# Kernel optimization log

Measured on AMD Instinct MI355X. Metric: run time of the kernel, lower is better.

The kernel has to match this reference:

```python
import jax, jax.numpy as jnp
import numpy as np

IN_C, OUT_C, K, STRIDE, PAD = 16, 32, 3, 1, 1


def setup_inputs() -> dict:
    key = jax.random.key(0)
    kx, kw = jax.random.split(key)
    x = jax.random.normal(kx, (2, IN_C, 8, 8, 32, 32), dtype=jnp.float32)
    # matches torch.randn init of nn.Parameter
    weight = jax.random.normal(kw, (OUT_C, IN_C, K, K, K, K), dtype=jnp.float32)
    bias = jnp.zeros((OUT_C,), dtype=jnp.float32)
    return {"x": x, "weight": weight, "bias": bias}


def _conv4d(x, weight):
    # 4 spatial dims; layout N C T D H W, weight O I kT kD kH kW.
    dn = jax.lax.ConvDimensionNumbers(
        lhs_spec=(0, 1, 2, 3, 4, 5),
        rhs_spec=(0, 1, 2, 3, 4, 5),
        out_spec=(0, 1, 2, 3, 4, 5),
    )
    return jax.lax.conv_general_dilated(
        x, weight,
        window_strides=(STRIDE,) * 4,
        padding=((PAD, PAD),) * 4,
        dimension_numbers=dn,
    )


def reference(x, weight, bias):
    # Same math as unfold(im2col) + matmul + bias in the torch module,
    # expressed as a single N-D convolution (implicit GEMM).
    out = _conv4d(x, weight)  # [B, out_c, oT, oD, oH, oW]
    return out + bias[None, :, None, None, None, None]
```

## Files before the change

### kernel.cpp

```cpp
#include <hip/hip_runtime.h>

#define IN_C  16
#define OUT_C 32
#define NB 2
#define TT 8
#define DD 8
#define HH 32
#define WW 32
#define TP 10
#define DP 10
#define HP 34
#define WPAD 34

#define XT_ROW_B  1088
#define XT_ELEMS  (NB*TP*DP*HP*2*WPAD*8)
#define WT_TAPS_P 84
#define WT_ELEMS  (WT_TAPS_P*2*OUT_C*8)

#define A_SLAB_B 12288
#define B_CHUNK_B 28672

typedef __bf16 bf16x8 __attribute__((ext_vector_type(8)));
typedef float  f32x4  __attribute__((ext_vector_type(4)));
typedef float  f32x16 __attribute__((ext_vector_type(16)));

__device__ __forceinline__ unsigned short f2bf(float f) {
    unsigned int u = __builtin_bit_cast(unsigned int, f);
    u += 0x7fffu + ((u >> 16) & 1u);
    return (unsigned short)(u >> 16);
}

__device__ __forceinline__ void gload16(const void* g, void* l) {
    __builtin_amdgcn_global_load_lds(
        (const __attribute__((address_space(1))) unsigned int*)g,
        (__attribute__((address_space(3))) unsigned int*)l, 16, 0, 0);
}

__global__ __launch_bounds__(256) void prep_kernel(const float* __restrict__ x,
                                                   const float* __restrict__ wsrc,
                                                   unsigned short* __restrict__ xt,
                                                   unsigned short* __restrict__ wt) {
    int b = blockIdx.x;
    int tid = threadIdx.x;
    if (b < 4096) {
        __shared__ unsigned short ls[WW * IN_C];
        int h = b & 31, d = (b >> 5) & 7, t = (b >> 8) & 7, n = b >> 11;
        int c = tid >> 5, w = tid & 31;
        float v0 = x[((((size_t)(n * IN_C + c)     * TT + t) * DD + d) * HH + h) * WW + w];
        float v1 = x[((((size_t)(n * IN_C + c + 8) * TT + t) * DD + d) * HH + h) * WW + w];
        ls[w * 16 + c]     = f2bf(v0);
        ls[w * 16 + c + 8] = f2bf(v1);
        __syncthreads();
        if (tid < 68) {
            int blk = tid / 34, wl = tid % 34;
            unsigned char* row = (unsigned char*)xt +
                (size_t)(((n * TP + t + 1) * DP + d + 1) * HP + h + 1) * XT_ROW_B;
            f32x4 val = {0.f, 0.f, 0.f, 0.f};
            if (wl != 0 && wl != 33)
                val = *(const f32x4*)((const unsigned char*)ls + (wl - 1) * 32 + blk * 16);
            *(f32x4*)(row + tid * 16) = val;
        }
    } else if (b < 6800) {
        int j = b - 4096;
        int n, tp, dp, hp;
        if (j < 1360)      { n = j / 680;  int r = j % 680;  tp = (r / 340) * 9; int r2 = r % 340; dp = r2 / 34;       hp = r2 % 34; }
        else if (j < 2448) { int j2 = j - 1360; n = j2 / 544; int r = j2 % 544; tp = 1 + r / 68;  int r3 = r % 68;  dp = (r3 / 34) * 9; hp = r3 % 34; }
        else               { int j3 = j - 2448; n = j3 / 128; int r = j3 % 128; tp = 1 + r / 16;  int r4 = r % 16;  dp = 1 + r4 / 2;   hp = (r4 & 1) * 33; }
        if (tid < 68) {
            unsigned char* row = (unsigned char*)xt +
                (size_t)(((n * TP + tp) * DP + dp) * HP + hp) * XT_ROW_B;
            f32x4 z = {0.f, 0.f, 0.f, 0.f};
            *(f32x4*)(row + tid * 16) = z;
        }
    } else {
        int idx = (b - 6800) * 256 + tid;
        int tap = idx >> 9;
        int r = idx & 511;
        int icblk = r >> 8, oc = (r >> 3) & 31, i8 = r & 7;
        int ic = icblk * 8 + i8;
        float v = (tap < 81) ? wsrc[(oc * IN_C + ic) * 81 + tap] : 0.0f;
        wt[idx] = f2bf(v);
    }
}

__global__ __launch_bounds__(256, 2) void conv_main_kernel(const unsigned short* __restrict__ xt,
                                                           const unsigned short* __restrict__ wt,
                                                           const float* __restrict__ bias,
                                                           float* __restrict__ out) {
    __shared__ __align__(16) unsigned char As0[A_SLAB_B];
    __shared__ __align__(16) unsigned char As1[A_SLAB_B];
    __shared__ __align__(16) unsigned char Bs0[B_CHUNK_B];
    __shared__ __align__(16) unsigned char Bs1[B_CHUNK_B];

    int bid = blockIdx.x;
    int lb  = (bid & 7) * 64 + (bid >> 3);
    int hb = lb & 3, d = (lb >> 2) & 7, t = (lb >> 5) & 7, n = lb >> 8;
    int h0 = hb * 8;
    int tid  = threadIdx.x;
    int wv   = tid >> 6;
    int lane = tid & 63;
    int l31  = lane & 31;
    int kblk = lane >> 5;

    int ab = kblk * 544 + l31 * 16;
    int bb = kblk * 512 + l31 * 16;

#pragma unroll
    for (int i = 0; i < 7; ++i)
        gload16((const unsigned char*)wt + (tid + i * 256) * 16, Bs0 + (tid + i * 256) * 16);
    {
        const unsigned char* src = (const unsigned char*)xt +
            (size_t)(((n * TP + t) * DP + d) * HP + h0) * XT_ROW_B;
#pragma unroll
        for (int i = 0; i < 3; ++i)
            gload16(src + (tid + i * 256) * 16, As0 + (tid + i * 256) * 16);
    }
    asm volatile("s_waitcnt vmcnt(0)" ::: "memory");
    __syncthreads();

    f32x16 acc[2];
    acc[0] = {}; acc[1] = {};

#pragma unroll
    for (int p = 0; p < 9; ++p) {
        const int kt = p / 3, ph3 = p % 3;

        if (p < 8) {
            const int ktn = (p + 1) / 3, kdn = (p + 1) % 3;
            const unsigned char* src = (const unsigned char*)xt +
                (size_t)(((n * TP + t + ktn) * DP + d + kdn) * HP + h0) * XT_ROW_B;
            unsigned char* dst = ((p + 1) & 1) ? As1 : As0;
#pragma unroll
            for (int i = 0; i < 3; ++i)
                gload16(src + (tid + i * 256) * 16, dst + (tid + i * 256) * 16);
        }
        const bool bstage = (kt < 2) && (ph3 <= 1);
        if (bstage) {
            const int basel = ph3 * 896;
            const unsigned char* bsrc = (const unsigned char*)wt +
                (size_t)((kt + 1) * 27 * 64 + basel) * 16;
            unsigned char* bdst = (((kt + 1) & 1) ? Bs1 : Bs0) + basel * 16;
#pragma unroll
            for (int i = 0; i < 3; ++i)
                gload16(bsrc + (tid + i * 256) * 16, bdst + (tid + i * 256) * 16);
            if (tid < 128)
                gload16(bsrc + (tid + 768) * 16, bdst + (tid + 768) * 16);
        }

        const unsigned char* A = (p & 1) ? As1 : As0;
        const unsigned char* B = (kt & 1) ? Bs1 : Bs0;
        const int kd = ph3;

        bf16x8 bf[3][3];
#pragma unroll
        for (int kh = 0; kh < 3; ++kh)
#pragma unroll
            for (int kw = 0; kw < 3; ++kw)
                bf[kh][kw] = *(const bf16x8*)(B + ((kd * 9 + kh * 3 + kw) << 10) + bb);

#pragma unroll
        for (int rr = 0; rr < 4; ++rr) {
#pragma unroll
            for (int kw = 0; kw < 3; ++kw) {
                bf16x8 a = *(const bf16x8*)(A + (2 * wv + rr) * 1088 + ab + kw * 16);
#pragma unroll
                for (int kh = 0; kh < 3; ++kh) {
                    const int m = rr - kh;
                    if (m >= 0 && m < 2)
                        acc[m] = __builtin_amdgcn_mfma_f32_32x32x16_bf16(a, bf[kh][kw], acc[m], 0, 0, 0);
                }
            }
        }

        if (bstage)
            asm volatile("s_waitcnt vmcnt(4)" ::: "memory");
        else
            asm volatile("s_waitcnt vmcnt(0)" ::: "memory");
        __syncthreads();
    }

    float bsv = bias[l31];
#pragma unroll
    for (int m = 0; m < 2; ++m) {
        int oh = h0 + 2 * wv + m;
        float* obase = out + (((((size_t)n * OUT_C + l31) * TT + t) * DD + d) * HH + oh) * WW;
#pragma unroll
        for (int q = 0; q < 4; ++q) {
            f32x4 v = { acc[m][4 * q + 0] + bsv, acc[m][4 * q + 1] + bsv,
                        acc[m][4 * q + 2] + bsv, acc[m][4 * q + 3] + bsv };
            *(f32x4*)(obase + 8 * q + 4 * kblk) = v;
        }
    }
}

extern "C" void kernel_launch(void* const* d_in, const int* in_sizes, int n_in,
                              void* d_out, int out_size, void* d_ws, size_t ws_size,
                              hipStream_t stream) {
    const float* x    = (const float*)d_in[0];
    const float* wsrc = (const float*)d_in[1];
    const float* bias = (const float*)d_in[2];
    float* out        = (float*)d_out;

    unsigned short* xt = (unsigned short*)d_ws;
    unsigned short* wt = xt + XT_ELEMS;

    prep_kernel<<<4096 + 2704 + 164, 256, 0, stream>>>(x, wsrc, xt, wt);
    conv_main_kernel<<<NB * TT * DD * 4, 256, 0, stream>>>(xt, wt, bias, out);
}
```

Baseline: 26.55 us.

## Load weights directly into registers and triple-buffer input slabs in LDS

Weight fragments are no longer staged through shared memory. Each wave now reads its bf16 weight fragments straight from global memory into a double-buffered register array, one phase ahead. The input slab buffers go from two to three, so A loads are prefetched two phases ahead and a single uniform s_waitcnt replaces the phase-dependent waits. This cuts LDS use and LDS traffic for B and gives global loads more time to land. In exchange it adds register pressure (18 bf16x8 fragments live) and per-wave global/L2 reads of the weights.

```diff
diff --git a/kernel.cpp b/kernel.cpp
--- a/kernel.cpp
+++ b/kernel.cpp
@@ -18,7 +18,6 @@
 #define WT_ELEMS  (WT_TAPS_P*2*OUT_C*8)
 
 #define A_SLAB_B 12288
-#define B_CHUNK_B 28672
 
 typedef __bf16 bf16x8 __attribute__((ext_vector_type(8)));
 typedef float  f32x4  __attribute__((ext_vector_type(4)));
@@ -87,10 +86,7 @@
                                                            const unsigned short* __restrict__ wt,
                                                            const float* __restrict__ bias,
                                                            float* __restrict__ out) {
-    __shared__ __align__(16) unsigned char As0[A_SLAB_B];
-    __shared__ __align__(16) unsigned char As1[A_SLAB_B];
-    __shared__ __align__(16) unsigned char Bs0[B_CHUNK_B];
-    __shared__ __align__(16) unsigned char Bs1[B_CHUNK_B];
+    __shared__ __align__(16) unsigned char As[3][A_SLAB_B];
 
     int bid = blockIdx.x;
     int lb  = (bid & 7) * 64 + (bid >> 3);
@@ -103,18 +99,26 @@
     int kblk = lane >> 5;
 
     int ab = kblk * 544 + l31 * 16;
-    int bb = kblk * 512 + l31 * 16;
+    const unsigned char* wb = (const unsigned char*)wt + kblk * 512 + l31 * 16;
 
+    auto asrc = [&](int p) {
+        return (const unsigned char*)xt +
+            (size_t)(((n * TP + t + p / 3) * DP + d + p % 3) * HP + h0) * XT_ROW_B;
+    };
+
+    {
+        const unsigned char* s0 = asrc(0);
+        const unsigned char* s1 = asrc(1);
 #pragma unroll
-    for (int i = 0; i < 7; ++i)
-        gload16((const unsigned char*)wt + (tid + i * 256) * 16, Bs0 + (tid + i * 256) * 16);
-    {
-        const unsigned char* src = (const unsigned char*)xt +
-            (size_t)(((n * TP + t) * DP + d) * HP + h0) * XT_ROW_B;
+        for (int i = 0; i < 3; ++i) {
+            gload16(s0 + (tid + i * 256) * 16, As[0] + (tid + i * 256) * 16);
+            gload16(s1 + (tid + i * 256) * 16, As[1] + (tid + i * 256) * 16);
+        }
+    }
+    bf16x8 bf[2][9];
 #pragma unroll
-        for (int i = 0; i < 3; ++i)
-            gload16(src + (tid + i * 256) * 16, As0 + (tid + i * 256) * 16);
-    }
+    for (int j = 0; j < 9; ++j)
+        bf[0][j] = *(const bf16x8*)(wb + (size_t)j * 1024);
     asm volatile("s_waitcnt vmcnt(0)" ::: "memory");
     __syncthreads();
 
@@ -123,41 +127,23 @@
 
 #pragma unroll
     for (int p = 0; p < 9; ++p) {
-        const int kt = p / 3, ph3 = p % 3;
+        const int cur = p & 1, nxt = cur ^ 1;
 
         if (p < 8) {
-            const int ktn = (p + 1) / 3, kdn = (p + 1) % 3;
-            const unsigned char* src = (const unsigned char*)xt +
-                (size_t)(((n * TP + t + ktn) * DP + d + kdn) * HP + h0) * XT_ROW_B;
-            unsigned char* dst = ((p + 1) & 1) ? As1 : As0;
+            const unsigned char* bsrc = wb + (size_t)(p + 1) * 9 * 1024;
+#pragma unroll
+            for (int j = 0; j < 9; ++j)
+                bf[nxt][j] = *(const bf16x8*)(bsrc + (size_t)j * 1024);
+        }
+        if (p < 7) {
+            const unsigned char* src = asrc(p + 2);
+            unsigned char* dst = As[(p + 2) % 3];
 #pragma unroll
             for (int i = 0; i < 3; ++i)
                 gload16(src + (tid + i * 256) * 16, dst + (tid + i * 256) * 16);
         }
-        const bool bstage = (kt < 2) && (ph3 <= 1);
-        if (bstage) {
-            const int basel = ph3 * 896;
-            const unsigned char* bsrc = (const unsigned char*)wt +
-                (size_t)((kt + 1) * 27 * 64 + basel) * 16;
-            unsigned char* bdst = (((kt + 1) & 1) ? Bs1 : Bs0) + basel * 16;
-#pragma unroll
-            for (int i = 0; i < 3; ++i)
-                gload16(bsrc + (tid + i * 256) * 16, bdst + (tid + i * 256) * 16);
-            if (tid < 128)
-                gload16(bsrc + (tid + 768) * 16, bdst + (tid + 768) * 16);
-        }
 
-        const unsigned char* A = (p & 1) ? As1 : As0;
-        const unsigned char* B = (kt & 1) ? Bs1 : Bs0;
-        const int kd = ph3;
-
-        bf16x8 bf[3][3];
-#pragma unroll
-        for (int kh = 0; kh < 3; ++kh)
-#pragma unroll
-            for (int kw = 0; kw < 3; ++kw)
-                bf[kh][kw] = *(const bf16x8*)(B + ((kd * 9 + kh * 3 + kw) << 10) + bb);
-
+        const unsigned char* A = As[p % 3];
 #pragma unroll
         for (int rr = 0; rr < 4; ++rr) {
 #pragma unroll
@@ -167,15 +153,12 @@
                 for (int kh = 0; kh < 3; ++kh) {
                     const int m = rr - kh;
                     if (m >= 0 && m < 2)
-                        acc[m] = __builtin_amdgcn_mfma_f32_32x32x16_bf16(a, bf[kh][kw], acc[m], 0, 0, 0);
+                        acc[m] = __builtin_amdgcn_mfma_f32_32x32x16_bf16(a, bf[cur][kh * 3 + kw], acc[m], 0, 0, 0);
                 }
             }
         }
 
-        if (bstage)
-            asm volatile("s_waitcnt vmcnt(4)" ::: "memory");
-        else
-            asm volatile("s_waitcnt vmcnt(0)" ::: "memory");
+        asm volatile("s_waitcnt vmcnt(3)" ::: "memory");
         __syncthreads();
     }
 
```

Result: slower. 29.54 us (+11.3%).
